# Performance work log

Measured on AMD Instinct MI355X. Metric: run time of the kernel, lower is better.

The kernel has to match this reference:

```python
import jax, jax.numpy as jnp
import numpy as np

H = 8            # num heads
K_ORDER = 3      # polynomial filter order


def setup_inputs() -> dict:
    key = jax.random.key(0)
    ks = jax.random.split(key, 7)
    B, N, D = 4, 2048, 256
    s = 0.05  # weight scale to keep softmax/poly numerically tame
    x = jax.random.normal(ks[0], (B, N, D), jnp.float32)
    Wq = jax.random.normal(ks[1], (D, D), jnp.float32) * s
    Wk = jax.random.normal(ks[2], (D, D), jnp.float32) * s
    Wv = jax.random.normal(ks[3], (D, D), jnp.float32) * s
    Wo = jax.random.normal(ks[4], (D, D), jnp.float32) * s
    coeffs = jax.random.normal(ks[5], (H, K_ORDER + 1), jnp.float32) * 0.5
    z = jnp.zeros((D,), jnp.float32)
    return {"x": x, "Wq": Wq, "bq": z, "Wk": Wk, "bk": z,
            "Wv": Wv, "bv": z, "Wo": Wo, "bo": z, "coeffs": coeffs}


def reference(x, Wq, bq, Wk, bk, Wv, bv, Wo, bo, coeffs):
    B, N, D = x.shape
    hd = D // H

    def split_heads(t):  # [B,N,D] -> [B,H,N,hd]
        return t.reshape(B, N, H, hd).transpose(0, 2, 1, 3)

    q = split_heads(x @ Wq + bq)
    k = split_heads(x @ Wk + bk)
    v = split_heads(x @ Wv + bv)

    # Estimator: learned adjacency via scaled-dot-product softmax, [B,H,N,N]
    scale = jnp.asarray(1.0 / np.sqrt(hd), x.dtype)
    A = jax.nn.softmax(jnp.einsum('bhnd,bhmd->bhnm', q, k) * scale, axis=-1)

    # Filter: X' = sum_{k=0}^{K} c[h,k] * A^k V
    out = coeffs[None, :, 0, None, None] * v
    t = v
    for kk in range(1, K_ORDER + 1):
        t = jnp.einsum('bhnm,bhmd->bhnd', A, t)
        out = out + coeffs[None, :, kk, None, None] * t

    merged = out.transpose(0, 2, 1, 3).reshape(B, N, D)  # concat heads
    return merged @ Wo + bo
```

## Files before the change

kernel.cpp:

```cpp
#include <hip/hip_runtime.h>
#include <hip/hip_bf16.h>

typedef __hip_bfloat16 bf16;
typedef __attribute__((ext_vector_type(8))) short short8;
typedef __attribute__((ext_vector_type(4))) short short4v;
typedef __attribute__((ext_vector_type(4))) float f32x4;

#define BB 4
#define NN 2048
#define DD 256
#define HH 8
#define HD 32
#define BN (BB*NN)
#define ELEMS (BN*DD)

__device__ int g_isf32;
__device__ __attribute__((aligned(256))) unsigned short g_xb [ELEMS];
__device__ __attribute__((aligned(256))) unsigned short g_qb [ELEMS];
__device__ __attribute__((aligned(256))) unsigned short g_kb [ELEMS];
__device__ __attribute__((aligned(256))) unsigned short g_tA [ELEMS];
__device__ __attribute__((aligned(256))) unsigned short g_tB [ELEMS];
__device__ __attribute__((aligned(256))) float          g_acc[ELEMS];
__device__ __attribute__((aligned(256))) unsigned short g_mg [ELEMS];
__device__ __attribute__((aligned(256))) unsigned short g_wt [4*DD*DD];
__device__ __attribute__((aligned(256))) float g_bias[4*DD];
__device__ __attribute__((aligned(256))) float g_cf[HH*4];
__device__ __attribute__((aligned(256))) float g_invl[BB*HH*NN];

__device__ __forceinline__ float b2f(unsigned short u) {
    union { unsigned int i; float f; } c; c.i = ((unsigned int)u) << 16; return c.f;
}
__device__ __forceinline__ unsigned short f2b(float f) {
    bf16 h = __float2bfloat16(f);
    return *reinterpret_cast<unsigned short*>(&h);
}
#if __has_builtin(__builtin_amdgcn_cvt_pk_bf16_f32)
typedef __attribute__((ext_vector_type(2))) __bf16 bf16x2t;
__device__ __forceinline__ unsigned int pk2(float a, float b) {
    union { bf16x2t v; unsigned int u; } c;
    c.v = __builtin_amdgcn_cvt_pk_bf16_f32(a, b);
    return c.u;
}
#else
__device__ __forceinline__ unsigned int pk2(float a, float b) {
    unsigned int ua = __float_as_uint(a), ub = __float_as_uint(b);
    ua = (ua + 0x7FFFu + ((ua >> 16) & 1u)) >> 16;
    ub = (ub + 0x7FFFu + ((ub >> 16) & 1u)) & 0xFFFF0000u;
    return ua | ub;
}
#endif
__device__ __forceinline__ float ldin(const void* p, int i, int f32m) {
    return f32m ? ((const float*)p)[i] : b2f(((const unsigned short*)p)[i]);
}

__global__ __launch_bounds__(256) void probe_kernel(const void* __restrict__ x)
{
    __shared__ int cnt;
    if (threadIdx.x == 0) cnt = 0;
    __syncthreads();
    const unsigned short* u = (const unsigned short*)x;
    int w = 0;
    for (int i = threadIdx.x; i < 1024; i += 256) {
        const int e = (u[2 * i] >> 7) & 0xFF;
        if (e < 100 || e > 140) ++w;
    }
    atomicAdd(&cnt, w);
    __syncthreads();
    if (threadIdx.x == 0) g_isf32 = (cnt > 300) ? 1 : 0;
}

__global__ __launch_bounds__(256) void prep_x_kernel(const void* __restrict__ x)
{
    const int f32m = g_isf32;
    const size_t i0 = ((size_t)blockIdx.x * 256 + threadIdx.x) * 8;
    if (f32m) {
        const float4 a = *(const float4*)((const float*)x + i0);
        const float4 b = *(const float4*)((const float*)x + i0 + 4);
        union { uint4 v; unsigned int u[4]; } o;
        o.u[0] = pk2(a.x, a.y); o.u[1] = pk2(a.z, a.w);
        o.u[2] = pk2(b.x, b.y); o.u[3] = pk2(b.z, b.w);
        *(uint4*)(g_xb + i0) = o.v;
    } else {
        *(uint4*)(g_xb + i0) = *(const uint4*)((const unsigned short*)x + i0);
    }
}

__global__ __launch_bounds__(256) void prep_w_kernel(
    const void* W0, const void* W1, const void* W2, const void* W3,
    const void* bq, const void* bk, const void* bv, const void* bo,
    const void* coeffs)
{
    const int f32m = g_isf32;
    __shared__ unsigned short tile[64][65];
    const int mat = blockIdx.y;
    const void* W = (mat == 0) ? W0 : (mat == 1) ? W1 : (mat == 2) ? W2 : W3;
    const int k0 = (blockIdx.x >> 2) * 64;
    const int n0 = (blockIdx.x & 3) * 64;
    const int t  = threadIdx.x;

    if (blockIdx.x == 0 && blockIdx.y == 0) {
        g_bias[0 * DD + t] = ldin(bq, t, f32m);
        g_bias[1 * DD + t] = ldin(bk, t, f32m);
        g_bias[2 * DD + t] = ldin(bv, t, f32m);
        g_bias[3 * DD + t] = ldin(bo, t, f32m);
        if (t < 32) g_cf[t] = ldin(coeffs, t, f32m);
    }

    #pragma unroll
    for (int it = 0; it < 16; ++it) {
        const int flat = it * 256 + t;
        const int i = flat >> 6, j = flat & 63;
        tile[j][i] = f2b(ldin(W, (k0 + i) * DD + n0 + j, f32m));
    }
    __syncthreads();
    unsigned short* wt = g_wt + mat * DD * DD;
    #pragma unroll
    for (int it = 0; it < 16; ++it) {
        const int flat = it * 256 + t;
        const int nl = flat >> 6, kl = flat & 63;
        wt[(n0 + nl) * DD + k0 + kl] = tile[nl][kl];
    }
}

__global__ __launch_bounds__(256) void qkv_gemm_kernel()
{
    __shared__ unsigned short xs[64 * 32];
    __shared__ unsigned short wl[64 * 32];
    const int t  = threadIdx.x;
    const int w  = t >> 6, l = t & 63, lg = l >> 4, ln = l & 15;
    const int r0 = blockIdx.x * 64;
    const int n0 = blockIdx.y * 64;
    const int mat = blockIdx.z;
    const unsigned short* wt = g_wt + mat * DD * DD;
    const int sr = t >> 2, sc = (t & 3) * 8;

    f32x4 acc[4] = {{0,0,0,0},{0,0,0,0},{0,0,0,0},{0,0,0,0}};

    for (int kc = 0; kc < DD; kc += 32) {
        __syncthreads();
        *(uint4*)(xs + sr * 32 + sc) =
            *(const uint4*)(g_xb + (size_t)(r0 + sr) * DD + kc + sc);
        *(uint4*)(wl + sr * 32 + sc) =
            *(const uint4*)(wt + (size_t)(n0 + sr) * DD + kc + sc);
        __syncthreads();
        const short8 af = *(const short8*)(xs + (w * 16 + ln) * 32 + lg * 8);
        #pragma unroll
        for (int s = 0; s < 4; ++s) {
            const short8 bfr = *(const short8*)(wl + (s * 16 + ln) * 32 + lg * 8);
            acc[s] = __builtin_amdgcn_mfma_f32_16x16x32_bf16(af, bfr, acc[s], 0, 0, 0);
        }
    }

    const float QS = 0.17677669529663687f * 1.4426950408889634f;
    #pragma unroll
    for (int s = 0; s < 4; ++s) {
        const int j = n0 + s * 16 + ln;
        const float bias = g_bias[mat * DD + j];
        const int h = j >> 5, dd = j & 31;
        #pragma unroll
        for (int r = 0; r < 4; ++r) {
            const int rn = r0 + w * 16 + lg * 4 + r;
            const int b = rn >> 11, n = rn & (NN - 1);
            const int bh = b * HH + h;
            const float val = acc[s][r] + bias;
            if (mat == 0) {
                g_qb[((size_t)bh * NN + n) * HD + dd] = f2b(val * QS);
            } else if (mat == 1) {
                g_kb[((size_t)bh * NN + n) * HD + dd] = f2b(val);
            } else {
                g_tA[((size_t)bh * HD + dd) * NN + n] = f2b(val);
                g_acc[(size_t)rn * DD + j] = g_cf[h * 4] * val;
            }
        }
    }
}

template<int KIND>
__global__ __launch_bounds__(256) void attn_pass_kernel(const int kidx, const int dir)
{
    __shared__ float osh[2][128][33];
    __shared__ float lsh[4][128];

    const unsigned short* __restrict__ tin  = dir ? g_tB : g_tA;
    unsigned short*       __restrict__ tout = dir ? g_tA : g_tB;

    const int tid = threadIdx.x;
    const int w   = tid >> 6;
    const int l   = tid & 63;
    const int lg  = l >> 4;
    const int ln  = l & 15;

    const int bi = blockIdx.x;
    const int bh = (bi & 7) * 4 + ((bi >> 3) & 3);
    const int qt = bi >> 5;
    const int h  = bh & (HH - 1);
    const int b  = bh >> 3;
    const int q0 = qt * 128;

    short8 qf[8];
    #pragma unroll
    for (int qi = 0; qi < 8; ++qi)
        qf[qi] = *(const short8*)(g_qb +
            ((size_t)bh * NN + q0 + qi * 16 + ln) * HD + lg * 8);

    const unsigned short* kb = g_kb + (size_t)bh * NN * HD;
    const unsigned short* tb = tin  + (size_t)bh * HD * NN;

    f32x4 oacc[8][2];
    #pragma unroll
    for (int qi = 0; qi < 8; ++qi) { oacc[qi][0] = (f32x4){0,0,0,0}; oacc[qi][1] = (f32x4){0,0,0,0}; }
    float lsum[8] = {0.f, 0.f, 0.f, 0.f, 0.f, 0.f, 0.f, 0.f};
    const f32x4 zero = {0.f, 0.f, 0.f, 0.f};

    for (int it = 0; it < 16; ++it) {
        const int k0 = it * 128 + w * 32;
        const short8 kf0 = *(const short8*)(kb + (size_t)(k0 + ln) * HD + lg * 8);
        const short8 kf1 = *(const short8*)(kb + (size_t)(k0 + 16 + ln) * HD + lg * 8);

#if __has_builtin(__builtin_amdgcn_mfma_f32_16x16x16bf16_1k)
        short4v tf[2][2];
        #pragma unroll
        for (int c = 0; c < 2; ++c)
            #pragma unroll
            for (int hf = 0; hf < 2; ++hf)
                tf[c][hf] = *(const short4v*)(tb +
                    (size_t)(hf * 16 + ln) * NN + k0 + c * 16 + lg * 4);

        #pragma unroll
        for (int qi = 0; qi < 8; ++qi) {
            f32x4 s0 = __builtin_amdgcn_mfma_f32_16x16x32_bf16(kf0, qf[qi], zero, 0, 0, 0);
            f32x4 s1 = __builtin_amdgcn_mfma_f32_16x16x32_bf16(kf1, qf[qi], zero, 0, 0, 0);
            float p[8];
            #pragma unroll
            for (int r = 0; r < 4; ++r) {
                p[r]     = __builtin_amdgcn_exp2f(s0[r]);
                p[4 + r] = __builtin_amdgcn_exp2f(s1[r]);
                if (KIND == 0) lsum[qi] += p[r] + p[4 + r];
            }
            union { unsigned int u[2]; short4v s; } pb0, pb1;
            pb0.u[0] = pk2(p[0], p[1]); pb0.u[1] = pk2(p[2], p[3]);
            pb1.u[0] = pk2(p[4], p[5]); pb1.u[1] = pk2(p[6], p[7]);
            oacc[qi][0] = __builtin_amdgcn_mfma_f32_16x16x16bf16_1k(tf[0][0], pb0.s, oacc[qi][0], 0, 0, 0);
            oacc[qi][1] = __builtin_amdgcn_mfma_f32_16x16x16bf16_1k(tf[0][1], pb0.s, oacc[qi][1], 0, 0, 0);
            oacc[qi][0] = __builtin_amdgcn_mfma_f32_16x16x16bf16_1k(tf[1][0], pb1.s, oacc[qi][0], 0, 0, 0);
            oacc[qi][1] = __builtin_amdgcn_mfma_f32_16x16x16bf16_1k(tf[1][1], pb1.s, oacc[qi][1], 0, 0, 0);
        }
#else
        const short8 tf0 = *(const short8*)(tb + (size_t)ln * NN + k0 + lg * 8);
        const short8 tf1 = *(const short8*)(tb + (size_t)(ln + 16) * NN + k0 + lg * 8);
        #pragma unroll
        for (int qi = 0; qi < 8; ++qi) {
            f32x4 s0 = __builtin_amdgcn_mfma_f32_16x16x32_bf16(kf0, qf[qi], zero, 0, 0, 0);
            f32x4 s1 = __builtin_amdgcn_mfma_f32_16x16x32_bf16(kf1, qf[qi], zero, 0, 0, 0);
            float p[8];
            #pragma unroll
            for (int r = 0; r < 4; ++r) {
                p[r]     = __builtin_amdgcn_exp2f(s0[r]);
                p[4 + r] = __builtin_amdgcn_exp2f(s1[r]);
                if (KIND == 0) lsum[qi] += p[r] + p[4 + r];
            }
            const unsigned int pk0 = pk2(p[0], p[1]);
            const unsigned int pk1 = pk2(p[2], p[3]);
            const unsigned int pk2v = pk2(p[4], p[5]);
            const unsigned int pk3 = pk2(p[6], p[7]);
            int bi2[4];
            #pragma unroll
            for (int j = 0; j < 4; ++j) {
                const int srcLane = (((2 * lg + (j >> 1)) & 3) << 4) + ln;
                const int lo = __shfl((j & 1) ? (int)pk1 : (int)pk0, srcLane, 64);
                const int hi = __shfl((j & 1) ? (int)pk3 : (int)pk2v, srcLane, 64);
                bi2[j] = (lg < 2) ? lo : hi;
            }
            union { int i[4]; short8 s; } pf;
            pf.i[0] = bi2[0]; pf.i[1] = bi2[1]; pf.i[2] = bi2[2]; pf.i[3] = bi2[3];
            oacc[qi][0] = __builtin_amdgcn_mfma_f32_16x16x32_bf16(tf0, pf.s, oacc[qi][0], 0, 0, 0);
            oacc[qi][1] = __builtin_amdgcn_mfma_f32_16x16x32_bf16(tf1, pf.s, oacc[qi][1], 0, 0, 0);
        }
#endif
    }

    if (KIND == 0) {
        #pragma unroll
        for (int qi = 0; qi < 8; ++qi) {
            lsum[qi] += __shfl_xor(lsum[qi], 16, 64);
            lsum[qi] += __shfl_xor(lsum[qi], 32, 64);
        }
        if (lg == 0) {
            #pragma unroll
            for (int qi = 0; qi < 8; ++qi) lsh[w][qi * 16 + ln] = lsum[qi];
        }
    }

    if (w < 2) {
        #pragma unroll
        for (int qi = 0; qi < 8; ++qi)
            #pragma unroll
            for (int hf = 0; hf < 2; ++hf)
                #pragma unroll
                for (int r = 0; r < 4; ++r)
                    osh[w][qi * 16 + ln][hf * 16 + lg * 4 + r] = oacc[qi][hf][r];
    }
    __syncthreads();
    if (w >= 2) {
        #pragma unroll
        for (int qi = 0; qi < 8; ++qi)
            #pragma unroll
            for (int hf = 0; hf < 2; ++hf)
                #pragma unroll
                for (int r = 0; r < 4; ++r)
                    osh[w - 2][qi * 16 + ln][hf * 16 + lg * 4 + r] += oacc[qi][hf][r];
    }
    __syncthreads();

    {
        const int q  = tid & 127;
        const int db = (tid >> 7) * 16;
        float invl;
        if (KIND == 0) {
            invl = 1.0f / (lsh[0][q] + lsh[1][q] + lsh[2][q] + lsh[3][q]);
            if (db == 0) g_invl[(size_t)bh * NN + q0 + q] = invl;
        } else {
            invl = g_invl[(size_t)bh * NN + q0 + q];
        }
        const float ck = g_cf[h * 4 + kidx];
        #pragma unroll
        for (int dd = 0; dd < 16; ++dd) {
            const int d = db + dd;
            const float val = (osh[0][q][d] + osh[1][q][d]) * invl;
            const size_t gi = ((size_t)(b * NN + q0 + q)) * DD + h * HD + d;
            if (KIND != 2) {
                tout[((size_t)bh * HD + d) * NN + q0 + q] = f2b(val);
                g_acc[gi] += ck * val;
            } else {
                g_mg[gi] = f2b(g_acc[gi] + ck * val);
            }
        }
    }
}

__global__ __launch_bounds__(256) void out_gemm_kernel(void* __restrict__ out)
{
    __shared__ unsigned short xs[64 * 32];
    __shared__ unsigned short wl[64 * 32];
    const int f32m = g_isf32;
    const int t  = threadIdx.x;
    const int w  = t >> 6, l = t & 63, lg = l >> 4, ln = l & 15;
    const int r0 = blockIdx.x * 64;
    const int n0 = blockIdx.y * 64;
    const unsigned short* wt = g_wt + 3 * DD * DD;
    const int sr = t >> 2, sc = (t & 3) * 8;

    f32x4 acc[4] = {{0,0,0,0},{0,0,0,0},{0,0,0,0},{0,0,0,0}};

    for (int kc = 0; kc < DD; kc += 32) {
        __syncthreads();
        *(uint4*)(xs + sr * 32 + sc) =
            *(const uint4*)(g_mg + (size_t)(r0 + sr) * DD + kc + sc);
        *(uint4*)(wl + sr * 32 + sc) =
            *(const uint4*)(wt + (size_t)(n0 + sr) * DD + kc + sc);
        __syncthreads();
        const short8 af = *(const short8*)(xs + (w * 16 + ln) * 32 + lg * 8);
        #pragma unroll
        for (int s = 0; s < 4; ++s) {
            const short8 bfr = *(const short8*)(wl + (s * 16 + ln) * 32 + lg * 8);
            acc[s] = __builtin_amdgcn_mfma_f32_16x16x32_bf16(af, bfr, acc[s], 0, 0, 0);
        }
    }

    #pragma unroll
    for (int s = 0; s < 4; ++s) {
        const int j = n0 + s * 16 + ln;
        const float bias = g_bias[3 * DD + j];
        #pragma unroll
        for (int r = 0; r < 4; ++r) {
            const int rn = r0 + w * 16 + lg * 4 + r;
            const float val = acc[s][r] + bias;
            if (f32m) ((float*)out)[(size_t)rn * DD + j] = val;
            else      ((bf16*)out)[(size_t)rn * DD + j] = __float2bfloat16(val);
        }
    }
}

extern "C" void kernel_launch(void* const* d_in, const int* in_sizes, int n_in,
                              void* d_out, int out_size, void* d_ws, size_t ws_size,
                              hipStream_t stream)
{
    const void* x      = d_in[0];
    const void* Wq     = d_in[1];
    const void* bq     = d_in[2];
    const void* Wk     = d_in[3];
    const void* bk     = d_in[4];
    const void* Wv     = d_in[5];
    const void* bv     = d_in[6];
    const void* Wo     = d_in[7];
    const void* bo     = d_in[8];
    const void* coeffs = d_in[9];
    (void)d_ws; (void)ws_size; (void)in_sizes; (void)n_in; (void)out_size;

    probe_kernel<<<1, 256, 0, stream>>>(x);

    prep_x_kernel<<<ELEMS / (256 * 8), 256, 0, stream>>>(x);
    prep_w_kernel<<<dim3(16, 4), 256, 0, stream>>>(Wq, Wk, Wv, Wo,
                                                   bq, bk, bv, bo, coeffs);

    qkv_gemm_kernel<<<dim3(128, 4, 3), 256, 0, stream>>>();

    const int agrid = (BB * HH) * (NN / 128);
    attn_pass_kernel<0><<<agrid, 256, 0, stream>>>(1, 0);
    attn_pass_kernel<1><<<agrid, 256, 0, stream>>>(2, 1);
    attn_pass_kernel<2><<<agrid, 256, 0, stream>>>(3, 0);

    out_gemm_kernel<<<dim3(128, 4), 256, 0, stream>>>(d_out);
}
```

Baseline: 226.5 us.

## Repartition attention passes by query rows with LDS-staged K and T tiles

Each attention pass now runs 512 threads (8 waves), and each wave owns 16 query rows and walks the whole key range. Before, 4 waves split the keys and reduced partial outputs through shared memory. Each 128-key tile of K and T is loaded cooperatively into padded LDS once per block and shared across waves, and the cross-wave output reduction and its two barriers are removed. The cost is two barriers per key tile, fewer independent MFMA chains per wave, and more LDS reads in the inner loop.

```diff
diff --git a/kernel.cpp b/kernel.cpp
--- a/kernel.cpp
+++ b/kernel.cpp
@@ -175,11 +175,13 @@
     }
 }
 
+#define KSP 40
+#define TSP 136
 template<int KIND>
-__global__ __launch_bounds__(256) void attn_pass_kernel(const int kidx, const int dir)
-{
-    __shared__ float osh[2][128][33];
-    __shared__ float lsh[4][128];
+__global__ __launch_bounds__(512) void attn_pass_kernel(const int kidx, const int dir)
+{
+    __shared__ unsigned short ks[128 * KSP];
+    __shared__ unsigned short ts[32 * TSP];
 
     const unsigned short* __restrict__ tin  = dir ? g_tB : g_tA;
     unsigned short*       __restrict__ tout = dir ? g_tA : g_tB;
@@ -196,140 +198,68 @@
     const int h  = bh & (HH - 1);
     const int b  = bh >> 3;
     const int q0 = qt * 128;
-
-    short8 qf[8];
-    #pragma unroll
-    for (int qi = 0; qi < 8; ++qi)
-        qf[qi] = *(const short8*)(g_qb +
-            ((size_t)bh * NN + q0 + qi * 16 + ln) * HD + lg * 8);
+    const int qw = q0 + w * 16;
+
+    const short8 qf = *(const short8*)(g_qb +
+        ((size_t)bh * NN + qw + ln) * HD + lg * 8);
 
     const unsigned short* kb = g_kb + (size_t)bh * NN * HD;
     const unsigned short* tb = tin  + (size_t)bh * HD * NN;
 
-    f32x4 oacc[8][2];
-    #pragma unroll
-    for (int qi = 0; qi < 8; ++qi) { oacc[qi][0] = (f32x4){0,0,0,0}; oacc[qi][1] = (f32x4){0,0,0,0}; }
-    float lsum[8] = {0.f, 0.f, 0.f, 0.f, 0.f, 0.f, 0.f, 0.f};
     const f32x4 zero = {0.f, 0.f, 0.f, 0.f};
+    f32x4 oacc0 = zero, oacc1 = zero;
+    float lsum = 0.f;
+
+    const int krow = tid >> 2, kcol = (tid & 3) * 8;
+    const int trow = tid >> 4, tcol = (tid & 15) * 8;
 
     for (int it = 0; it < 16; ++it) {
-        const int k0 = it * 128 + w * 32;
-        const short8 kf0 = *(const short8*)(kb + (size_t)(k0 + ln) * HD + lg * 8);
-        const short8 kf1 = *(const short8*)(kb + (size_t)(k0 + 16 + ln) * HD + lg * 8);
-
-#if __has_builtin(__builtin_amdgcn_mfma_f32_16x16x16bf16_1k)
-        short4v tf[2][2];
-        #pragma unroll
-        for (int c = 0; c < 2; ++c)
+        const int k0 = it * 128;
+        __syncthreads();
+        *(uint4*)(ks + krow * KSP + kcol) =
+            *(const uint4*)(kb + (size_t)k0 * HD + tid * 8);
+        *(uint4*)(ts + trow * TSP + tcol) =
+            *(const uint4*)(tb + (size_t)trow * NN + k0 + tcol);
+        __syncthreads();
+
+        #pragma unroll
+        for (int c = 0; c < 8; ++c) {
+            const short8 kf = *(const short8*)(ks + (c * 16 + ln) * KSP + lg * 8);
+            f32x4 s = __builtin_amdgcn_mfma_f32_16x16x32_bf16(kf, qf, zero, 0, 0, 0);
+            float p[4];
             #pragma unroll
-            for (int hf = 0; hf < 2; ++hf)
-                tf[c][hf] = *(const short4v*)(tb +
-                    (size_t)(hf * 16 + ln) * NN + k0 + c * 16 + lg * 4);
-
-        #pragma unroll
-        for (int qi = 0; qi < 8; ++qi) {
-            f32x4 s0 = __builtin_amdgcn_mfma_f32_16x16x32_bf16(kf0, qf[qi], zero, 0, 0, 0);
-            f32x4 s1 = __builtin_amdgcn_mfma_f32_16x16x32_bf16(kf1, qf[qi], zero, 0, 0, 0);
-            float p[8];
-            #pragma unroll
-            for (int r = 0; r < 4; ++r) {
-                p[r]     = __builtin_amdgcn_exp2f(s0[r]);
-                p[4 + r] = __builtin_amdgcn_exp2f(s1[r]);
-                if (KIND == 0) lsum[qi] += p[r] + p[4 + r];
-            }
-            union { unsigned int u[2]; short4v s; } pb0, pb1;
-            pb0.u[0] = pk2(p[0], p[1]); pb0.u[1] = pk2(p[2], p[3]);
-            pb1.u[0] = pk2(p[4], p[5]); pb1.u[1] = pk2(p[6], p[7]);
-            oacc[qi][0] = __builtin_amdgcn_mfma_f32_16x16x16bf16_1k(tf[0][0], pb0.s, oacc[qi][0], 0, 0, 0);
-            oacc[qi][1] = __builtin_amdgcn_mfma_f32_16x16x16bf16_1k(tf[0][1], pb0.s, oacc[qi][1], 0, 0, 0);
-            oacc[qi][0] = __builtin_amdgcn_mfma_f32_16x16x16bf16_1k(tf[1][0], pb1.s, oacc[qi][0], 0, 0, 0);
-            oacc[qi][1] = __builtin_amdgcn_mfma_f32_16x16x16bf16_1k(tf[1][1], pb1.s, oacc[qi][1], 0, 0, 0);
-        }
-#else
-        const short8 tf0 = *(const short8*)(tb + (size_t)ln * NN + k0 + lg * 8);
-        const short8 tf1 = *(const short8*)(tb + (size_t)(ln + 16) * NN + k0 + lg * 8);
-        #pragma unroll
-        for (int qi = 0; qi < 8; ++qi) {
-            f32x4 s0 = __builtin_amdgcn_mfma_f32_16x16x32_bf16(kf0, qf[qi], zero, 0, 0, 0);
-            f32x4 s1 = __builtin_amdgcn_mfma_f32_16x16x32_bf16(kf1, qf[qi], zero, 0, 0, 0);
-            float p[8];
-            #pragma unroll
-            for (int r = 0; r < 4; ++r) {
-                p[r]     = __builtin_amdgcn_exp2f(s0[r]);
-                p[4 + r] = __builtin_amdgcn_exp2f(s1[r]);
-                if (KIND == 0) lsum[qi] += p[r] + p[4 + r];
-            }
-            const unsigned int pk0 = pk2(p[0], p[1]);
-            const unsigned int pk1 = pk2(p[2], p[3]);
-            const unsigned int pk2v = pk2(p[4], p[5]);
-            const unsigned int pk3 = pk2(p[6], p[7]);
-            int bi2[4];
-            #pragma unroll
-            for (int j = 0; j < 4; ++j) {
-                const int srcLane = (((2 * lg + (j >> 1)) & 3) << 4) + ln;
-                const int lo = __shfl((j & 1) ? (int)pk1 : (int)pk0, srcLane, 64);
-                const int hi = __shfl((j & 1) ? (int)pk3 : (int)pk2v, srcLane, 64);
-                bi2[j] = (lg < 2) ? lo : hi;
-            }
-            union { int i[4]; short8 s; } pf;
-            pf.i[0] = bi2[0]; pf.i[1] = bi2[1]; pf.i[2] = bi2[2]; pf.i[3] = bi2[3];
-            oacc[qi][0] = __builtin_amdgcn_mfma_f32_16x16x32_bf16(tf0, pf.s, oacc[qi][0], 0, 0, 0);
-            oacc[qi][1] = __builtin_amdgcn_mfma_f32_16x16x32_bf16(tf1, pf.s, oacc[qi][1], 0, 0, 0);
-        }
-#endif
-    }
-
+            for (int r = 0; r < 4; ++r) p[r] = __builtin_amdgcn_exp2f(s[r]);
+            if (KIND == 0) lsum += p[0] + p[1] + p[2] + p[3];
+            union { unsigned int u[2]; short4v s4; } pb;
+            pb.u[0] = pk2(p[0], p[1]); pb.u[1] = pk2(p[2], p[3]);
+            const short4v tf0 = *(const short4v*)(ts + ln * TSP + c * 16 + lg * 4);
+            const short4v tf1 = *(const short4v*)(ts + (16 + ln) * TSP + c * 16 + lg * 4);
+            oacc0 = __builtin_amdgcn_mfma_f32_16x16x16bf16_1k(tf0, pb.s4, oacc0, 0, 0, 0);
+            oacc1 = __builtin_amdgcn_mfma_f32_16x16x16bf16_1k(tf1, pb.s4, oacc1, 0, 0, 0);
+        }
+    }
+
+    float invl;
     if (KIND == 0) {
-        #pragma unroll
-        for (int qi = 0; qi < 8; ++qi) {
-            lsum[qi] += __shfl_xor(lsum[qi], 16, 64);
-            lsum[qi] += __shfl_xor(lsum[qi], 32, 64);
-        }
-        if (lg == 0) {
-            #pragma unroll
-            for (int qi = 0; qi < 8; ++qi) lsh[w][qi * 16 + ln] = lsum[qi];
-        }
-    }
-
-    if (w < 2) {
-        #pragma unroll
-        for (int qi = 0; qi < 8; ++qi)
-            #pragma unroll
-            for (int hf = 0; hf < 2; ++hf)
-                #pragma unroll
-                for (int r = 0; r < 4; ++r)
-                    osh[w][qi * 16 + ln][hf * 16 + lg * 4 + r] = oacc[qi][hf][r];
-    }
-    __syncthreads();
-    if (w >= 2) {
-        #pragma unroll
-        for (int qi = 0; qi < 8; ++qi)
-            #pragma unroll
-            for (int hf = 0; hf < 2; ++hf)
-                #pragma unroll
-                for (int r = 0; r < 4; ++r)
-                    osh[w - 2][qi * 16 + ln][hf * 16 + lg * 4 + r] += oacc[qi][hf][r];
-    }
-    __syncthreads();
-
-    {
-        const int q  = tid & 127;
-        const int db = (tid >> 7) * 16;
-        float invl;
-        if (KIND == 0) {
-            invl = 1.0f / (lsh[0][q] + lsh[1][q] + lsh[2][q] + lsh[3][q]);
-            if (db == 0) g_invl[(size_t)bh * NN + q0 + q] = invl;
-        } else {
-            invl = g_invl[(size_t)bh * NN + q0 + q];
-        }
-        const float ck = g_cf[h * 4 + kidx];
-        #pragma unroll
-        for (int dd = 0; dd < 16; ++dd) {
-            const int d = db + dd;
-            const float val = (osh[0][q][d] + osh[1][q][d]) * invl;
-            const size_t gi = ((size_t)(b * NN + q0 + q)) * DD + h * HD + d;
+        lsum += __shfl_xor(lsum, 16, 64);
+        lsum += __shfl_xor(lsum, 32, 64);
+        invl = 1.0f / lsum;
+        if (lg == 0) g_invl[(size_t)bh * NN + qw + ln] = invl;
+    } else {
+        invl = g_invl[(size_t)bh * NN + qw + ln];
+    }
+
+    const float ck = g_cf[h * 4 + kidx];
+    #pragma unroll
+    for (int hf = 0; hf < 2; ++hf) {
+        const f32x4& oa = hf ? oacc1 : oacc0;
+        #pragma unroll
+        for (int r = 0; r < 4; ++r) {
+            const int d = hf * 16 + lg * 4 + r;
+            const float val = oa[r] * invl;
+            const size_t gi = ((size_t)(b * NN + qw + ln)) * DD + h * HD + d;
             if (KIND != 2) {
-                tout[((size_t)bh * HD + d) * NN + q0 + q] = f2b(val);
+                tout[((size_t)bh * HD + d) * NN + qw + ln] = f2b(val);
                 g_acc[gi] += ck * val;
             } else {
                 g_mg[gi] = f2b(g_acc[gi] + ck * val);
@@ -406,9 +336,9 @@
     qkv_gemm_kernel<<<dim3(128, 4, 3), 256, 0, stream>>>();
 
     const int agrid = (BB * HH) * (NN / 128);
-    attn_pass_kernel<0><<<agrid, 256, 0, stream>>>(1, 0);
-    attn_pass_kernel<1><<<agrid, 256, 0, stream>>>(2, 1);
-    attn_pass_kernel<2><<<agrid, 256, 0, stream>>>(3, 0);
+    attn_pass_kernel<0><<<agrid, 512, 0, stream>>>(1, 0);
+    attn_pass_kernel<1><<<agrid, 512, 0, stream>>>(2, 1);
+    attn_pass_kernel<2><<<agrid, 512, 0, stream>>>(3, 0);
 
     out_gemm_kernel<<<dim3(128, 4), 256, 0, stream>>>(d_out);
 }
```

After: 226.7 us. Within noise of the previous version (+0.1%).
